# Kernel tuning notes

Hardware: AMD Instinct MI355X
Metric: run time of the kernel (lower is better)

The kernel has to match this reference:

```python
import jax, jax.numpy as jnp
import numpy as np

SIGMAS = [1.0, 2.0, 4.0, 8.0, 16.0]
EPS = 0.05
ITERS = 30
N, M, D = 8192, 8192, 128


def _sqdist(X, Y):
    # ||x_i - y_j||^2, [n, m]
    d2 = (jnp.sum(X * X, axis=1)[:, None]
          + jnp.sum(Y * Y, axis=1)[None, :]
          - 2.0 * (X @ Y.T))
    return jnp.maximum(d2, 0.0)


def _ms_rbf(X, Y):
    d2 = _sqdist(X, Y)
    K = jnp.zeros_like(d2)
    for s in SIGMAS:  # small fixed loop over scales
        K = K + jnp.exp(-d2 / (2.0 * s * s))
    return K / float(len(SIGMAS))


def _sinkhorn_uniform(cost, eps, iters):
    n, m = cost.shape
    dtype = cost.dtype
    log_a = jnp.asarray(-np.log(float(n)), dtype)
    log_b = jnp.asarray(-np.log(float(m)), dtype)
    log_K = -(cost - jax.lax.stop_gradient(jnp.min(cost))) / eps

    def step(carry, _):
        log_u, log_v = carry
        log_u = log_a - jax.scipy.special.logsumexp(log_K + log_v[None, :], axis=1)
        log_v = log_b - jax.scipy.special.logsumexp(log_K + log_u[:, None], axis=0)
        return (log_u, log_v), None

    init = (jnp.zeros((n,), dtype), jnp.zeros((m,), dtype))
    (log_u, log_v), _ = jax.lax.scan(step, init, None, length=iters)
    return jnp.exp(log_u[:, None] + log_K + log_v[None, :])


def setup_inputs() -> dict:
    key = jax.random.key(0)
    kx, ky = jax.random.split(key)
    X = jax.random.normal(kx, (N, D), dtype=jnp.float32)
    Y = jax.random.normal(ky, (M, D), dtype=jnp.float32)
    return {"X": X, "Y": Y}


def reference(X, Y):
    Kxx = jnp.mean(_ms_rbf(X, X))
    Kyy = jnp.mean(_ms_rbf(Y, Y))
    Kxy = _ms_rbf(X, Y)
    cost = 1.0 / float(X.shape[0] * Y.shape[0]) - Kxy
    Gamma = _sinkhorn_uniform(cost, EPS, ITERS)
    Kxy_weighted = jnp.sum(Gamma * Kxy)
    return Kxx + Kyy - 2.0 * Kxy_weighted
```

## Files before the change

kernel.cpp:

```cpp
#include <hip/hip_runtime.h>
#include <math.h>

#define NR 8192
#define DDIM 128

static constexpr float LOG_AB2      = -13.0f;
static constexpr float INV_EPS      = 20.0f;
static constexpr float L2E          = 1.4426950408889634f;
static constexpr float INV_EPS_L2E  = 28.853900817779268f;
static constexpr float C8           = 0.11315255222658537f;
static constexpr float DQK8         = 1.0f / 255.0f;
static constexpr float E1 = -0.7213475204444817f;
static constexpr float E2 = -0.18033688011112043f;
static constexpr float E3 = -0.045084220027780107f;
static constexpr float E4 = -0.011271055006945027f;
static constexpr float E5 = -0.0028177637517362567f;

#if defined(__has_builtin)
#if __has_builtin(__builtin_amdgcn_exp2f)
#define EX2_IMPL(x) __builtin_amdgcn_exp2f(x)
#endif
#endif
#ifndef EX2_IMPL
extern "C" __device__ float __ocml_native_exp2_f32(float);
#define EX2_IMPL(x) __ocml_native_exp2_f32(x)
#endif
__device__ inline float ex2(float x) { return EX2_IMPL(x); }


__global__ __launch_bounds__(256) void rownorm_k(const float* __restrict__ X,
                                                 float* __restrict__ nrm) {
    const int lane = threadIdx.x & 63;
    const int w    = threadIdx.x >> 6;
    const int row  = blockIdx.x * 4 + w;
    const float2 v = *reinterpret_cast<const float2*>(&X[(size_t)row * DDIM + lane * 2]);
    float s = v.x * v.x + v.y * v.y;
#pragma unroll
    for (int off = 32; off; off >>= 1) s += __shfl_xor(s, off);
    if (lane == 0) nrm[row] = s;
}

template <int MODE>
__global__ __launch_bounds__(256) void gemm_rbf_k(const float* __restrict__ Xp,
                                                  const float* __restrict__ Yp,
                                                  const float* __restrict__ nxp,
                                                  const float* __restrict__ nyp,
                                                  unsigned char* __restrict__ K8,
                                                  unsigned* __restrict__ maxbits,
                                                  double* __restrict__ sums) {
    int bm, bn;
    const float *A, *B, *na, *nb;
    if (MODE == 0) {
        bm = blockIdx.x; bn = blockIdx.y;
        A = Xp; B = Yp; na = nxp; nb = nyp;
    } else {
        const int lin = blockIdx.x;
        int i = (int)((129.0f - sqrtf(16641.0f - 8.0f * (float)lin)) * 0.5f);
        while (i * 64 - i * (i - 1) / 2 > lin) --i;
        while ((i + 1) * 64 - (i + 1) * i / 2 <= lin) ++i;
        bm = i;
        bn = i + (lin - (i * 64 - i * (i - 1) / 2));
        const int sel = blockIdx.y;
        A = B = sel ? Yp : Xp;
        na = nb = sel ? nyp : nxp;
    }
    __shared__ float As[32 * 128];
    __shared__ float Bs[32 * 128];
    __shared__ float redmax[4];
    const int t   = threadIdx.x;
    const int row = t & 127;
    const int kh  = t >> 7;
    const float* Arow = &A[(size_t)(bm * 128 + row) * DDIM];
    const float* Brow = &B[(size_t)(bn * 128 + row) * DDIM];
    const int tx = t & 15, ty = t >> 4;

    float acc[8][8];
#pragma unroll
    for (int i = 0; i < 8; ++i)
#pragma unroll
        for (int j = 0; j < 8; ++j) acc[i][j] = 0.f;

    for (int kc = 0; kc < 4; ++kc) {
        __syncthreads();
#pragma unroll
        for (int p = 0; p < 4; ++p) {
            const int k4 = kh + 2 * p;
            const float4 va = *reinterpret_cast<const float4*>(&Arow[kc * 32 + k4 * 4]);
            As[(4 * k4 + 0) * 128 + row] = va.x;
            As[(4 * k4 + 1) * 128 + row] = va.y;
            As[(4 * k4 + 2) * 128 + row] = va.z;
            As[(4 * k4 + 3) * 128 + row] = va.w;
            const float4 vb = *reinterpret_cast<const float4*>(&Brow[kc * 32 + k4 * 4]);
            Bs[(4 * k4 + 0) * 128 + row] = vb.x;
            Bs[(4 * k4 + 1) * 128 + row] = vb.y;
            Bs[(4 * k4 + 2) * 128 + row] = vb.z;
            Bs[(4 * k4 + 3) * 128 + row] = vb.w;
        }
        __syncthreads();
#pragma unroll 8
        for (int k = 0; k < 32; ++k) {
            const float4 a0 = *reinterpret_cast<const float4*>(&As[k * 128 + ty * 4]);
            const float4 a1 = *reinterpret_cast<const float4*>(&As[k * 128 + 64 + ty * 4]);
            const float4 b0 = *reinterpret_cast<const float4*>(&Bs[k * 128 + tx * 4]);
            const float4 b1 = *reinterpret_cast<const float4*>(&Bs[k * 128 + 64 + tx * 4]);
            const float a[8] = {a0.x, a0.y, a0.z, a0.w, a1.x, a1.y, a1.z, a1.w};
            const float b[8] = {b0.x, b0.y, b0.z, b0.w, b1.x, b1.y, b1.z, b1.w};
#pragma unroll
            for (int i = 0; i < 8; ++i)
#pragma unroll
                for (int j = 0; j < 8; ++j) acc[i][j] = fmaf(a[i], b[j], acc[i][j]);
        }
    }

    const int m0 = bm * 128, n0 = bn * 128;
    float nbv[8];
#pragma unroll
    for (int j = 0; j < 8; ++j) nbv[j] = nb[n0 + tx * 4 + (j & 3) + (j >> 2) * 64];

    float  lmax = 0.f;
    double lsum = 0.0;
#pragma unroll
    for (int i = 0; i < 8; ++i) {
        const int   mi  = m0 + ty * 4 + (i & 3) + (i >> 2) * 64;
        const float nav = na[mi];
        float kv[8];
#pragma unroll
        for (int j = 0; j < 8; ++j) {
            float d2 = fmaf(-2.f, acc[i][j], nav + nbv[j]);
            d2 = fmaxf(d2, 0.f);
            kv[j] = 0.2f * (ex2(d2 * E1) + ex2(d2 * E2) + ex2(d2 * E3) +
                            ex2(d2 * E4) + ex2(d2 * E5));
        }
        if (MODE == 0) {
            uchar4 o0, o1;
            o0.x = (unsigned char)__float2uint_rn(kv[0] * 255.f);
            o0.y = (unsigned char)__float2uint_rn(kv[1] * 255.f);
            o0.z = (unsigned char)__float2uint_rn(kv[2] * 255.f);
            o0.w = (unsigned char)__float2uint_rn(kv[3] * 255.f);
            o1.x = (unsigned char)__float2uint_rn(kv[4] * 255.f);
            o1.y = (unsigned char)__float2uint_rn(kv[5] * 255.f);
            o1.z = (unsigned char)__float2uint_rn(kv[6] * 255.f);
            o1.w = (unsigned char)__float2uint_rn(kv[7] * 255.f);
            *reinterpret_cast<uchar4*>(&K8[(size_t)mi * NR + n0 + tx * 4])      = o0;
            *reinterpret_cast<uchar4*>(&K8[(size_t)mi * NR + n0 + 64 + tx * 4]) = o1;
#pragma unroll
            for (int j = 0; j < 8; ++j) lmax = fmaxf(lmax, kv[j]);
        } else {
#pragma unroll
            for (int j = 0; j < 8; ++j) lsum += (double)kv[j];
        }
    }
    if (MODE == 0) {
#pragma unroll
        for (int off = 32; off; off >>= 1) lmax = fmaxf(lmax, __shfl_xor(lmax, off));
        if ((t & 63) == 0) redmax[t >> 6] = lmax;
        __syncthreads();
        if (t == 0) {
            lmax = fmaxf(fmaxf(redmax[0], redmax[1]), fmaxf(redmax[2], redmax[3]));
            atomicMax(maxbits, __float_as_uint(lmax));
        }
    } else {
        if (bn > bm) lsum *= 2.0;
#pragma unroll
        for (int off = 32; off; off >>= 1) lsum += __shfl_xor(lsum, off);
        if ((t & 63) == 0) atomicAdd(&sums[1 + blockIdx.y], lsum);
    }
}

__global__ __launch_bounds__(256) void init_lv_k(float* __restrict__ log_v,
                                                 const unsigned* __restrict__ scal_u) {
    const float kmax = __uint_as_float(scal_u[0]);
    log_v[blockIdx.x * 256 + threadIdx.x] = -kmax * INV_EPS_L2E;
}

__global__ __launch_bounds__(256) void sink_row_k(const unsigned char* __restrict__ K8,
                                                  const float* __restrict__ log_v,
                                                  float* __restrict__ log_u,
                                                  const unsigned* __restrict__ scal_u) {
    __shared__ float red[4][8];
    const int t  = threadIdx.x;
    const int r0 = blockIdx.x * 8;
    const float off2 = -__uint_as_float(scal_u[0]) * INV_EPS_L2E;
    const float4* Lv4 = reinterpret_cast<const float4*>(log_v);
    float s[8];
#pragma unroll
    for (int r = 0; r < 8; ++r) s[r] = 0.f;
#pragma unroll
    for (int p = 0; p < 2; ++p) {
        const int g = t + p * 256;
        const float4 l0 = Lv4[4 * g + 0];
        const float4 l1 = Lv4[4 * g + 1];
        const float4 l2 = Lv4[4 * g + 2];
        const float4 l3 = Lv4[4 * g + 3];
        const float lvv[16] = {l0.x, l0.y, l0.z, l0.w, l1.x, l1.y, l1.z, l1.w,
                               l2.x, l2.y, l2.z, l2.w, l3.x, l3.y, l3.z, l3.w};
        const uint4* col = reinterpret_cast<const uint4*>(K8 + (size_t)r0 * NR) + g;
#pragma unroll
        for (int r = 0; r < 8; ++r) {
            const uint4 w = col[(size_t)r * 512];
            const unsigned wd[4] = {w.x, w.y, w.z, w.w};
#pragma unroll
            for (int d = 0; d < 4; ++d) {
                const unsigned a = wd[d];
                s[r] += ex2(fmaf((float)(a & 255u),          C8, lvv[4 * d + 0]))
                      + ex2(fmaf((float)((a >> 8) & 255u),   C8, lvv[4 * d + 1]))
                      + ex2(fmaf((float)((a >> 16) & 255u),  C8, lvv[4 * d + 2]))
                      + ex2(fmaf((float)(a >> 24),           C8, lvv[4 * d + 3]));
            }
        }
    }
    const int lane = t & 63, w = t >> 6;
#pragma unroll
    for (int r = 0; r < 8; ++r) {
        float v = s[r];
#pragma unroll
        for (int o = 32; o; o >>= 1) v += __shfl_xor(v, o);
        if (lane == 0) red[w][r] = v;
    }
    __syncthreads();
    if (t < 8) {
        const float stot = (red[0][t] + red[1][t]) + (red[2][t] + red[3][t]);
        log_u[r0 + t] = LOG_AB2 - __log2f(stot) + off2;
    }
}

__global__ __launch_bounds__(256) void sink_colp_k(const unsigned char* __restrict__ K8,
                                                   const float* __restrict__ log_u,
                                                   float* __restrict__ ps) {
    const int t  = threadIdx.x;
    const int cg = blockIdx.x * 256 + t;
    const int rc = blockIdx.y;
    const uint4* base = reinterpret_cast<const uint4*>(K8) + (size_t)rc * 32 * 512 + cg;
    const float* lu = log_u + rc * 32;
    float s16[16];
#pragma unroll
    for (int e = 0; e < 16; ++e) s16[e] = 0.f;
#pragma unroll 4
    for (int r = 0; r < 32; ++r) {
        const uint4 w = base[(size_t)r * 512];
        const float lur = lu[r];
        const unsigned wd[4] = {w.x, w.y, w.z, w.w};
#pragma unroll
        for (int d = 0; d < 4; ++d) {
            const unsigned a = wd[d];
            s16[4 * d + 0] += ex2(fmaf((float)(a & 255u),         C8, lur));
            s16[4 * d + 1] += ex2(fmaf((float)((a >> 8) & 255u),  C8, lur));
            s16[4 * d + 2] += ex2(fmaf((float)((a >> 16) & 255u), C8, lur));
            s16[4 * d + 3] += ex2(fmaf((float)(a >> 24),          C8, lur));
        }
    }
    float4* pv = reinterpret_cast<float4*>(ps + (size_t)rc * NR + cg * 16);
#pragma unroll
    for (int d = 0; d < 4; ++d)
        pv[d] = {s16[4 * d + 0], s16[4 * d + 1], s16[4 * d + 2], s16[4 * d + 3]};
}

__global__ __launch_bounds__(256) void sink_combine_k(const float* __restrict__ ps,
                                                      float* __restrict__ log_v,
                                                      const unsigned* __restrict__ scal_u) {
    __shared__ float red[4][64];
    const int lane = threadIdx.x & 63;
    const int grp  = threadIdx.x >> 6;
    const int col  = blockIdx.x * 64 + lane;
    float s = 0.f;
#pragma unroll 8
    for (int c = grp * 64; c < grp * 64 + 64; ++c) s += ps[(size_t)c * NR + col];
    red[grp][lane] = s;
    __syncthreads();
    if (grp == 0) {
        const float stot = (red[0][lane] + red[1][lane]) + (red[2][lane] + red[3][lane]);
        const float off2 = -__uint_as_float(scal_u[0]) * INV_EPS_L2E;
        log_v[col] = LOG_AB2 - __log2f(stot) + off2;
    }
}

__global__ __launch_bounds__(256) void gamma_sum_k(const unsigned char* __restrict__ K8,
                                                   const float* __restrict__ log_u,
                                                   const float* __restrict__ log_v,
                                                   const unsigned* __restrict__ scal_u,
                                                   double* __restrict__ S) {
    const int t  = threadIdx.x;
    const int cg = blockIdx.x * 256 + t;
    const int rc = blockIdx.y;
    const float off2 = -__uint_as_float(scal_u[0]) * INV_EPS_L2E;
    float lvp[16];
#pragma unroll
    for (int e = 0; e < 16; ++e) lvp[e] = log_v[cg * 16 + e] - off2;
    const uint4* base = reinterpret_cast<const uint4*>(K8) + (size_t)rc * 32 * 512 + cg;
    const float* lu = log_u + rc * 32;
    double acc = 0.0;
#pragma unroll 4
    for (int r = 0; r < 32; ++r) {
        const uint4 w = base[(size_t)r * 512];
        const float lur = lu[r];
        const unsigned wd[4] = {w.x, w.y, w.z, w.w};
        float rs = 0.f;
#pragma unroll
        for (int d = 0; d < 4; ++d) {
            const unsigned a = wd[d];
            const float q0 = (float)(a & 255u);
            const float q1 = (float)((a >> 8) & 255u);
            const float q2 = (float)((a >> 16) & 255u);
            const float q3 = (float)(a >> 24);
            rs = fmaf(ex2(fmaf(q0, C8, lur + lvp[4 * d + 0])), q0, rs);
            rs = fmaf(ex2(fmaf(q1, C8, lur + lvp[4 * d + 1])), q1, rs);
            rs = fmaf(ex2(fmaf(q2, C8, lur + lvp[4 * d + 2])), q2, rs);
            rs = fmaf(ex2(fmaf(q3, C8, lur + lvp[4 * d + 3])), q3, rs);
        }
        acc += (double)rs;
    }
#pragma unroll
    for (int o = 32; o; o >>= 1) acc += __shfl_xor(acc, o);
    if ((t & 63) == 0) atomicAdd(S, acc);
}

__global__ void finalize_k(const double* __restrict__ scal, float* __restrict__ out) {
    const double inv = 1.0 / (8192.0 * 8192.0);
    out[0] = (float)(scal[1] * inv + scal[2] * inv - 2.0 * (double)DQK8 * scal[3]);
}

extern "C" void kernel_launch(void* const* d_in, const int* in_sizes, int n_in,
                              void* d_out, int out_size, void* d_ws, size_t ws_size,
                              hipStream_t stream) {
    const float* X = (const float*)d_in[0];
    const float* Y = (const float*)d_in[1];

    char* ws = (char*)d_ws;
    unsigned char* K8 = (unsigned char*)ws;
    float* nx    = (float*)(ws + 67108864);
    float* ny    = nx + NR;
    float* log_u = ny + NR;
    float* log_v = log_u + NR;
    char*  scal  = (char*)(log_v + NR);
    unsigned* scal_u = (unsigned*)scal;
    double*   scal_d = (double*)scal;
    float* ps = (float*)(scal + 512);
    const size_t needed = 67108864 + 4 * (size_t)NR * 4 + 512 + 256 * (size_t)NR * 4;
    if (ws_size < needed) return;

    hipMemsetAsync(scal, 0, 512, stream);

    rownorm_k<<<NR / 4, 256, 0, stream>>>(X, nx);
    rownorm_k<<<NR / 4, 256, 0, stream>>>(Y, ny);

    gemm_rbf_k<0><<<dim3(64, 64), 256, 0, stream>>>(X, Y, nx, ny, K8, scal_u, scal_d);
    gemm_rbf_k<1><<<dim3(2080, 2), 256, 0, stream>>>(X, Y, nx, ny, nullptr, scal_u, scal_d);

    init_lv_k<<<NR / 256, 256, 0, stream>>>(log_v, scal_u);

    for (int it = 0; it < 30; ++it) {
        sink_row_k<<<NR / 8, 256, 0, stream>>>(K8, log_v, log_u, scal_u);
        sink_colp_k<<<dim3(2, 256), 256, 0, stream>>>(K8, log_u, ps);
        sink_combine_k<<<128, 256, 0, stream>>>(ps, log_v, scal_u);
    }

    gamma_sum_k<<<dim3(2, 256), 256, 0, stream>>>(K8, log_u, log_v, scal_u, scal_d + 3);
    finalize_k<<<1, 1, 0, stream>>>(scal_d, (float*)d_out);
}
```

Measured before the change: 1.768 ms.

## Replace FP32 FMA GEMM with split-bf16 MFMA GEMM and drop kmax reduction

Both input matrices are pre-split into bf16 high and low parts. The distance GEMMs now run on 16x16x32 bf16 MFMA instructions, using three products (hi*hi, hi*lo, lo*hi) to approximate FP32 accuracy. This replaces the scalar FMA outer-product loop. The global atomicMax for the kernel maximum is also removed and the log-domain shift is hardcoded to a constant, which mathematically cancels in Sinkhorn. In exchange, the change adds conversion kernels and extra workspace, and the epilogue now writes single bytes instead of packed uchar4 stores.

New measurement: 1.603 ms. -9.3%, faster.

```diff
diff --git a/kernel.cpp b/kernel.cpp
--- a/kernel.cpp
+++ b/kernel.cpp
@@ -4,17 +4,18 @@
 #define NR 8192
 #define DDIM 128
 
-static constexpr float LOG_AB2      = -13.0f;
-static constexpr float INV_EPS      = 20.0f;
-static constexpr float L2E          = 1.4426950408889634f;
-static constexpr float INV_EPS_L2E  = 28.853900817779268f;
-static constexpr float C8           = 0.11315255222658537f;
-static constexpr float DQK8         = 1.0f / 255.0f;
+static constexpr float LOG_AB2 = -13.0f;
+static constexpr float OFF2    = -28.853900817779268f;
+static constexpr float C8      = 0.11315255222658537f;
+static constexpr float DQK8    = 1.0f / 255.0f;
 static constexpr float E1 = -0.7213475204444817f;
 static constexpr float E2 = -0.18033688011112043f;
 static constexpr float E3 = -0.045084220027780107f;
 static constexpr float E4 = -0.011271055006945027f;
 static constexpr float E5 = -0.0028177637517362567f;
+
+typedef __attribute__((ext_vector_type(8))) short  s16x8;
+typedef __attribute__((ext_vector_type(4))) float  f32x4;
 
 #if defined(__has_builtin)
 #if __has_builtin(__builtin_amdgcn_exp2f)
@@ -27,6 +28,31 @@
 #endif
 __device__ inline float ex2(float x) { return EX2_IMPL(x); }
 
+__device__ inline unsigned short bf16rn(float f) {
+    const unsigned u = __float_as_uint(f);
+    return (unsigned short)((u + 0x7FFFu + ((u >> 16) & 1u)) >> 16);
+}
+
+__global__ __launch_bounds__(256) void conv_k(const float* __restrict__ X,
+                                              unsigned short* __restrict__ hi,
+                                              unsigned short* __restrict__ lo) {
+    const int i = blockIdx.x * 1024 + threadIdx.x * 4;
+    const float4 v = *reinterpret_cast<const float4*>(&X[i]);
+    const float f[4] = {v.x, v.y, v.z, v.w};
+    ushort4 h, l;
+    unsigned short hh[4], ll[4];
+#pragma unroll
+    for (int j = 0; j < 4; ++j) {
+        const unsigned short a = bf16rn(f[j]);
+        const float hf = __uint_as_float((unsigned)a << 16);
+        hh[j] = a;
+        ll[j] = bf16rn(f[j] - hf);
+    }
+    h.x = hh[0]; h.y = hh[1]; h.z = hh[2]; h.w = hh[3];
+    l.x = ll[0]; l.y = ll[1]; l.z = ll[2]; l.w = ll[3];
+    *reinterpret_cast<ushort4*>(&hi[i]) = h;
+    *reinterpret_cast<ushort4*>(&lo[i]) = l;
+}
 
 __global__ __launch_bounds__(256) void rownorm_k(const float* __restrict__ X,
                                                  float* __restrict__ nrm) {
@@ -41,18 +67,20 @@
 }
 
 template <int MODE>
-__global__ __launch_bounds__(256) void gemm_rbf_k(const float* __restrict__ Xp,
-                                                  const float* __restrict__ Yp,
-                                                  const float* __restrict__ nxp,
-                                                  const float* __restrict__ nyp,
-                                                  unsigned char* __restrict__ K8,
-                                                  unsigned* __restrict__ maxbits,
-                                                  double* __restrict__ sums) {
+__global__ __launch_bounds__(256) void gemm_mfma_k(const unsigned short* __restrict__ XH,
+                                                   const unsigned short* __restrict__ XL,
+                                                   const unsigned short* __restrict__ YH,
+                                                   const unsigned short* __restrict__ YL,
+                                                   const float* __restrict__ nxp,
+                                                   const float* __restrict__ nyp,
+                                                   unsigned char* __restrict__ K8,
+                                                   double* __restrict__ sums) {
     int bm, bn;
-    const float *A, *B, *na, *nb;
+    const unsigned short *AH, *AL, *BH, *BL;
+    const float *na, *nb;
     if (MODE == 0) {
         bm = blockIdx.x; bn = blockIdx.y;
-        A = Xp; B = Yp; na = nxp; nb = nyp;
+        AH = XH; AL = XL; BH = YH; BL = YL; na = nxp; nb = nyp;
     } else {
         const int lin = blockIdx.x;
         int i = (int)((129.0f - sqrtf(16641.0f - 8.0f * (float)lin)) * 0.5f);
@@ -61,126 +89,126 @@
         bm = i;
         bn = i + (lin - (i * 64 - i * (i - 1) / 2));
         const int sel = blockIdx.y;
-        A = B = sel ? Yp : Xp;
+        AH = BH = sel ? YH : XH;
+        AL = BL = sel ? YL : XL;
         na = nb = sel ? nyp : nxp;
     }
-    __shared__ float As[32 * 128];
-    __shared__ float Bs[32 * 128];
-    __shared__ float redmax[4];
-    const int t   = threadIdx.x;
-    const int row = t & 127;
-    const int kh  = t >> 7;
-    const float* Arow = &A[(size_t)(bm * 128 + row) * DDIM];
-    const float* Brow = &B[(size_t)(bn * 128 + row) * DDIM];
-    const int tx = t & 15, ty = t >> 4;
-
-    float acc[8][8];
-#pragma unroll
-    for (int i = 0; i < 8; ++i)
-#pragma unroll
-        for (int j = 0; j < 8; ++j) acc[i][j] = 0.f;
+    __shared__ unsigned short AsH[128 * 40], AsL[128 * 40], BsH[128 * 40], BsL[128 * 40];
+
+    const int t    = threadIdx.x;
+    const int lane = t & 63;
+    const int w    = t >> 6;
+    const int wr   = w >> 1, wc = w & 1;
+    const int l15  = lane & 15, lg = lane >> 4;
+
+    f32x4 acc[4][4];
+#pragma unroll
+    for (int mi = 0; mi < 4; ++mi)
+#pragma unroll
+        for (int ni = 0; ni < 4; ++ni) acc[mi][ni] = (f32x4){0.f, 0.f, 0.f, 0.f};
+
+    const unsigned short* gAH = AH + (size_t)(bm * 128) * DDIM;
+    const unsigned short* gAL = AL + (size_t)(bm * 128) * DDIM;
+    const unsigned short* gBH = BH + (size_t)(bn * 128) * DDIM;
+    const unsigned short* gBL = BL + (size_t)(bn * 128) * DDIM;
 
     for (int kc = 0; kc < 4; ++kc) {
+        const int k0 = kc * 32;
         __syncthreads();
 #pragma unroll
-        for (int p = 0; p < 4; ++p) {
-            const int k4 = kh + 2 * p;
-            const float4 va = *reinterpret_cast<const float4*>(&Arow[kc * 32 + k4 * 4]);
-            As[(4 * k4 + 0) * 128 + row] = va.x;
-            As[(4 * k4 + 1) * 128 + row] = va.y;
-            As[(4 * k4 + 2) * 128 + row] = va.z;
-            As[(4 * k4 + 3) * 128 + row] = va.w;
-            const float4 vb = *reinterpret_cast<const float4*>(&Brow[kc * 32 + k4 * 4]);
-            Bs[(4 * k4 + 0) * 128 + row] = vb.x;
-            Bs[(4 * k4 + 1) * 128 + row] = vb.y;
-            Bs[(4 * k4 + 2) * 128 + row] = vb.z;
-            Bs[(4 * k4 + 3) * 128 + row] = vb.w;
+        for (int q = 0; q < 2; ++q) {
+            const int idx = t + q * 256;
+            const int row = idx >> 2, seg = idx & 3;
+            const int go = row * DDIM + k0 + seg * 8;
+            const int so = row * 40 + seg * 8;
+            *reinterpret_cast<uint4*>(&AsH[so]) = *reinterpret_cast<const uint4*>(&gAH[go]);
+            *reinterpret_cast<uint4*>(&AsL[so]) = *reinterpret_cast<const uint4*>(&gAL[go]);
+            *reinterpret_cast<uint4*>(&BsH[so]) = *reinterpret_cast<const uint4*>(&gBH[go]);
+            *reinterpret_cast<uint4*>(&BsL[so]) = *reinterpret_cast<const uint4*>(&gBL[go]);
         }
         __syncthreads();
-#pragma unroll 8
-        for (int k = 0; k < 32; ++k) {
-            const float4 a0 = *reinterpret_cast<const float4*>(&As[k * 128 + ty * 4]);
-            const float4 a1 = *reinterpret_cast<const float4*>(&As[k * 128 + 64 + ty * 4]);
-            const float4 b0 = *reinterpret_cast<const float4*>(&Bs[k * 128 + tx * 4]);
-            const float4 b1 = *reinterpret_cast<const float4*>(&Bs[k * 128 + 64 + tx * 4]);
-            const float a[8] = {a0.x, a0.y, a0.z, a0.w, a1.x, a1.y, a1.z, a1.w};
-            const float b[8] = {b0.x, b0.y, b0.z, b0.w, b1.x, b1.y, b1.z, b1.w};
-#pragma unroll
-            for (int i = 0; i < 8; ++i)
-#pragma unroll
-                for (int j = 0; j < 8; ++j) acc[i][j] = fmaf(a[i], b[j], acc[i][j]);
-        }
-    }
-
-    const int m0 = bm * 128, n0 = bn * 128;
-    float nbv[8];
-#pragma unroll
-    for (int j = 0; j < 8; ++j) nbv[j] = nb[n0 + tx * 4 + (j & 3) + (j >> 2) * 64];
-
-    float  lmax = 0.f;
-    double lsum = 0.0;
-#pragma unroll
-    for (int i = 0; i < 8; ++i) {
-        const int   mi  = m0 + ty * 4 + (i & 3) + (i >> 2) * 64;
-        const float nav = na[mi];
-        float kv[8];
-#pragma unroll
-        for (int j = 0; j < 8; ++j) {
-            float d2 = fmaf(-2.f, acc[i][j], nav + nbv[j]);
-            d2 = fmaxf(d2, 0.f);
-            kv[j] = 0.2f * (ex2(d2 * E1) + ex2(d2 * E2) + ex2(d2 * E3) +
-                            ex2(d2 * E4) + ex2(d2 * E5));
-        }
-        if (MODE == 0) {
-            uchar4 o0, o1;
-            o0.x = (unsigned char)__float2uint_rn(kv[0] * 255.f);
-            o0.y = (unsigned char)__float2uint_rn(kv[1] * 255.f);
-            o0.z = (unsigned char)__float2uint_rn(kv[2] * 255.f);
-            o0.w = (unsigned char)__float2uint_rn(kv[3] * 255.f);
-            o1.x = (unsigned char)__float2uint_rn(kv[4] * 255.f);
-            o1.y = (unsigned char)__float2uint_rn(kv[5] * 255.f);
-            o1.z = (unsigned char)__float2uint_rn(kv[6] * 255.f);
-            o1.w = (unsigned char)__float2uint_rn(kv[7] * 255.f);
-            *reinterpret_cast<uchar4*>(&K8[(size_t)mi * NR + n0 + tx * 4])      = o0;
-            *reinterpret_cast<uchar4*>(&K8[(size_t)mi * NR + n0 + 64 + tx * 4]) = o1;
-#pragma unroll
-            for (int j = 0; j < 8; ++j) lmax = fmaxf(lmax, kv[j]);
-        } else {
-#pragma unroll
-            for (int j = 0; j < 8; ++j) lsum += (double)kv[j];
-        }
-    }
+
+        s16x8 bh[4], bl[4];
+#pragma unroll
+        for (int ni = 0; ni < 4; ++ni) {
+            const int off = (wc * 64 + ni * 16 + l15) * 40 + lg * 8;
+            bh[ni] = *reinterpret_cast<const s16x8*>(&BsH[off]);
+            bl[ni] = *reinterpret_cast<const s16x8*>(&BsL[off]);
+        }
+#pragma unroll
+        for (int mi = 0; mi < 4; ++mi) {
+            const int off = (wr * 64 + mi * 16 + l15) * 40 + lg * 8;
+            const s16x8 ah = *reinterpret_cast<const s16x8*>(&AsH[off]);
+            const s16x8 al = *reinterpret_cast<const s16x8*>(&AsL[off]);
+#pragma unroll
+            for (int ni = 0; ni < 4; ++ni) {
+                acc[mi][ni] = __builtin_amdgcn_mfma_f32_16x16x32_bf16(ah, bh[ni], acc[mi][ni], 0, 0, 0);
+                acc[mi][ni] = __builtin_amdgcn_mfma_f32_16x16x32_bf16(ah, bl[ni], acc[mi][ni], 0, 0, 0);
+                acc[mi][ni] = __builtin_amdgcn_mfma_f32_16x16x32_bf16(al, bh[ni], acc[mi][ni], 0, 0, 0);
+            }
+        }
+    }
+
+    const int mBase = bm * 128 + wr * 64;
+    const int nBase = bn * 128 + wc * 64;
+    float nbv[4];
+#pragma unroll
+    for (int ni = 0; ni < 4; ++ni) nbv[ni] = nb[nBase + ni * 16 + l15];
+
     if (MODE == 0) {
 #pragma unroll
-        for (int off = 32; off; off >>= 1) lmax = fmaxf(lmax, __shfl_xor(lmax, off));
-        if ((t & 63) == 0) redmax[t >> 6] = lmax;
-        __syncthreads();
-        if (t == 0) {
-            lmax = fmaxf(fmaxf(redmax[0], redmax[1]), fmaxf(redmax[2], redmax[3]));
-            atomicMax(maxbits, __float_as_uint(lmax));
+        for (int mi = 0; mi < 4; ++mi) {
+#pragma unroll
+            for (int j = 0; j < 4; ++j) {
+                const int m = mBase + mi * 16 + lg * 4 + j;
+                const float nav = na[m];
+                unsigned char* krow = &K8[(size_t)m * NR + nBase + l15];
+#pragma unroll
+                for (int ni = 0; ni < 4; ++ni) {
+                    float d2 = fmaf(-2.f, acc[mi][ni][j], nav + nbv[ni]);
+                    d2 = fmaxf(d2, 0.f);
+                    const float kv = 0.2f * (ex2(d2 * E1) + ex2(d2 * E2) + ex2(d2 * E3) +
+                                             ex2(d2 * E4) + ex2(d2 * E5));
+                    krow[ni * 16] = (unsigned char)__float2uint_rn(kv * 255.f);
+                }
+            }
         }
     } else {
+        double lsum = 0.0;
+#pragma unroll
+        for (int mi = 0; mi < 4; ++mi) {
+#pragma unroll
+            for (int j = 0; j < 4; ++j) {
+                const int m = mBase + mi * 16 + lg * 4 + j;
+                const float nav = na[m];
+                float rs = 0.f;
+#pragma unroll
+                for (int ni = 0; ni < 4; ++ni) {
+                    float d2 = fmaf(-2.f, acc[mi][ni][j], nav + nbv[ni]);
+                    d2 = fmaxf(d2, 0.f);
+                    rs += 0.2f * (ex2(d2 * E1) + ex2(d2 * E2) + ex2(d2 * E3) +
+                                  ex2(d2 * E4) + ex2(d2 * E5));
+                }
+                lsum += (double)rs;
+            }
+        }
         if (bn > bm) lsum *= 2.0;
 #pragma unroll
-        for (int off = 32; off; off >>= 1) lsum += __shfl_xor(lsum, off);
-        if ((t & 63) == 0) atomicAdd(&sums[1 + blockIdx.y], lsum);
-    }
-}
-
-__global__ __launch_bounds__(256) void init_lv_k(float* __restrict__ log_v,
-                                                 const unsigned* __restrict__ scal_u) {
-    const float kmax = __uint_as_float(scal_u[0]);
-    log_v[blockIdx.x * 256 + threadIdx.x] = -kmax * INV_EPS_L2E;
+        for (int o = 32; o; o >>= 1) lsum += __shfl_xor(lsum, o);
+        if (lane == 0) atomicAdd(&sums[1 + blockIdx.y], lsum);
+    }
+}
+
+__global__ __launch_bounds__(256) void init_lv_k(float* __restrict__ log_v) {
+    log_v[blockIdx.x * 256 + threadIdx.x] = OFF2;
 }
 
 __global__ __launch_bounds__(256) void sink_row_k(const unsigned char* __restrict__ K8,
                                                   const float* __restrict__ log_v,
-                                                  float* __restrict__ log_u,
-                                                  const unsigned* __restrict__ scal_u) {
+                                                  float* __restrict__ log_u) {
     __shared__ float red[4][8];
     const int t  = threadIdx.x;
     const int r0 = blockIdx.x * 8;
-    const float off2 = -__uint_as_float(scal_u[0]) * INV_EPS_L2E;
     const float4* Lv4 = reinterpret_cast<const float4*>(log_v);
     float s[8];
 #pragma unroll
@@ -220,7 +248,7 @@
     __syncthreads();
     if (t < 8) {
         const float stot = (red[0][t] + red[1][t]) + (red[2][t] + red[3][t]);
-        log_u[r0 + t] = LOG_AB2 - __log2f(stot) + off2;
+        log_u[r0 + t] = LOG_AB2 - __log2f(stot) + OFF2;
     }
 }
 
@@ -256,8 +284,7 @@
 }
 
 __global__ __launch_bounds__(256) void sink_combine_k(const float* __restrict__ ps,
-                                                      float* __restrict__ log_v,
-                                                      const unsigned* __restrict__ scal_u) {
+                                                      float* __restrict__ log_v) {
     __shared__ float red[4][64];
     const int lane = threadIdx.x & 63;
     const int grp  = threadIdx.x >> 6;
@@ -269,23 +296,20 @@
     __syncthreads();
     if (grp == 0) {
         const float stot = (red[0][lane] + red[1][lane]) + (red[2][lane] + red[3][lane]);
-        const float off2 = -__uint_as_float(scal_u[0]) * INV_EPS_L2E;
-        log_v[col] = LOG_AB2 - __log2f(stot) + off2;
+        log_v[col] = LOG_AB2 - __log2f(stot) + OFF2;
     }
 }
 
 __global__ __launch_bounds__(256) void gamma_sum_k(const unsigned char* __restrict__ K8,
                                                    const float* __restrict__ log_u,
                                                    const float* __restrict__ log_v,
-                                                   const unsigned* __restrict__ scal_u,
                                                    double* __restrict__ S) {
     const int t  = threadIdx.x;
     const int cg = blockIdx.x * 256 + t;
     const int rc = blockIdx.y;
-    const float off2 = -__uint_as_float(scal_u[0]) * INV_EPS_L2E;
     float lvp[16];
 #pragma unroll
-    for (int e = 0; e < 16; ++e) lvp[e] = log_v[cg * 16 + e] - off2;
+    for (int e = 0; e < 16; ++e) lvp[e] = log_v[cg * 16 + e] - OFF2;
     const uint4* base = reinterpret_cast<const uint4*>(K8) + (size_t)rc * 32 * 512 + cg;
     const float* lu = log_u + rc * 32;
     double acc = 0.0;
@@ -332,28 +356,33 @@
     float* log_u = ny + NR;
     float* log_v = log_u + NR;
     char*  scal  = (char*)(log_v + NR);
-    unsigned* scal_u = (unsigned*)scal;
-    double*   scal_d = (double*)scal;
+    double* scal_d = (double*)scal;
     float* ps = (float*)(scal + 512);
-    const size_t needed = 67108864 + 4 * (size_t)NR * 4 + 512 + 256 * (size_t)NR * 4;
+    unsigned short* XH = (unsigned short*)(ws + 75629056);
+    unsigned short* XL = XH + NR * DDIM;
+    unsigned short* YH = XL + NR * DDIM;
+    unsigned short* YL = YH + NR * DDIM;
+    const size_t needed = 75629056 + 4 * (size_t)NR * DDIM * 2;
     if (ws_size < needed) return;
 
     hipMemsetAsync(scal, 0, 512, stream);
 
+    conv_k<<<NR * DDIM / 1024, 256, 0, stream>>>(X, XH, XL);
+    conv_k<<<NR * DDIM / 1024, 256, 0, stream>>>(Y, YH, YL);
     rownorm_k<<<NR / 4, 256, 0, stream>>>(X, nx);
     rownorm_k<<<NR / 4, 256, 0, stream>>>(Y, ny);
 
-    gemm_rbf_k<0><<<dim3(64, 64), 256, 0, stream>>>(X, Y, nx, ny, K8, scal_u, scal_d);
-    gemm_rbf_k<1><<<dim3(2080, 2), 256, 0, stream>>>(X, Y, nx, ny, nullptr, scal_u, scal_d);
-
-    init_lv_k<<<NR / 256, 256, 0, stream>>>(log_v, scal_u);
+    gemm_mfma_k<0><<<dim3(64, 64), 256, 0, stream>>>(XH, XL, YH, YL, nx, ny, K8, scal_d);
+    gemm_mfma_k<1><<<dim3(2080, 2), 256, 0, stream>>>(XH, XL, YH, YL, nx, ny, nullptr, scal_d);
+
+    init_lv_k<<<NR / 256, 256, 0, stream>>>(log_v);
 
     for (int it = 0; it < 30; ++it) {
-        sink_row_k<<<NR / 8, 256, 0, stream>>>(K8, log_v, log_u, scal_u);
+        sink_row_k<<<NR / 8, 256, 0, stream>>>(K8, log_v, log_u);
         sink_colp_k<<<dim3(2, 256), 256, 0, stream>>>(K8, log_u, ps);
-        sink_combine_k<<<128, 256, 0, stream>>>(ps, log_v, scal_u);
-    }
-
-    gamma_sum_k<<<dim3(2, 256), 256, 0, stream>>>(K8, log_u, log_v, scal_u, scal_d + 3);
+        sink_combine_k<<<128, 256, 0, stream>>>(ps, log_v);
+    }
+
+    gamma_sum_k<<<dim3(2, 256), 256, 0, stream>>>(K8, log_u, log_v, scal_d + 3);
     finalize_k<<<1, 1, 0, stream>>>(scal_d, (float*)d_out);
 }
```
